# Optimization experiments

Measured on AMD Instinct MI355X. Metric: run time of the kernel, lower is better.

Reference implementation:

```python
import jax, jax.numpy as jnp
import numpy as np

B, T, C = 2, 2048, 2048
H, KV, D = 16, 4, 128   # n_head, n_kv_head, head_dim
EPS = 1.1920929e-07     # torch.finfo(float32).eps, F.rms_norm default


def setup_inputs() -> dict:
    key = jax.random.key(0)
    ks = jax.random.split(key, 7)
    x = jax.random.normal(ks[0], (B, T, C), dtype=jnp.float32)
    # rope angles: cos/sin of positions, broadcastable to [B,T,H,D//2]
    inv_freq = 1.0 / (10000.0 ** (jnp.arange(0, D // 2, dtype=jnp.float32) / (D // 2)))
    ang = jnp.arange(T, dtype=jnp.float32)[:, None] * inv_freq[None, :]
    cos = jnp.cos(ang)[None, :, None, :]  # [1,T,1,D/2]
    sin = jnp.sin(ang)[None, :, None, :]
    s = 0.02
    Wq = jax.random.normal(ks[1], (C, H * D), dtype=jnp.float32) * s
    Wk = jax.random.normal(ks[2], (C, KV * D), dtype=jnp.float32) * s
    Wv = jax.random.normal(ks[3], (C, KV * D), dtype=jnp.float32) * s
    Wo = jax.random.normal(ks[4], (C, C), dtype=jnp.float32) * s
    return {"x": x, "cos": cos, "sin": sin, "Wq": Wq, "Wk": Wk, "Wv": Wv, "Wo": Wo}


def _rope(t, cos, sin):
    d = t.shape[-1] // 2
    t1, t2 = t[..., :d], t[..., d:]
    return jnp.concatenate([t1 * cos + t2 * sin, -t1 * sin + t2 * cos], axis=-1)


def _rmsnorm(t):
    return t * jax.lax.rsqrt(jnp.mean(t * t, axis=-1, keepdims=True) + EPS)


def reference(x, cos, sin, Wq, Wk, Wv, Wo):
    q = (x @ Wq).reshape(B, T, H, D)
    k = (x @ Wk).reshape(B, T, KV, D)
    v = (x @ Wv).reshape(B, T, KV, D)
    q = _rmsnorm(_rope(q, cos, sin))
    k = _rmsnorm(_rope(k, cos, sin))
    # [B, KV, G, T, D] query grouped per kv head (GQA)
    G = H // KV
    qh = q.transpose(0, 2, 1, 3).reshape(B, KV, G, T, D)
    kh = k.transpose(0, 2, 1, 3)  # [B, KV, T, D]
    vh = v.transpose(0, 2, 1, 3)
    scale = 1.0 / np.sqrt(D).astype(np.float32)
    scores = jnp.einsum('bhgqd,bhkd->bhgqk', qh, kh) * scale
    causal = jnp.tril(jnp.ones((T, T), dtype=bool))
    scores = jnp.where(causal, scores, jnp.finfo(scores.dtype).min)
    attn = jax.nn.softmax(scores, axis=-1)
    y = jnp.einsum('bhgqk,bhkd->bhgqd', attn, vh)  # [B,KV,G,T,D]
    y = y.reshape(B, H, T, D).transpose(0, 2, 1, 3).reshape(B, T, C)
    return y @ Wo
```

## Files before the change

### kernel.cpp

```cpp
#include <hip/hip_runtime.h>

using bf16x8 = __attribute__((ext_vector_type(8))) short;
using f32x4  = __attribute__((ext_vector_type(4))) float;

#define B_  2
#define T_  2048
#define C_  2048
#define H_  16
#define KV_ 4
#define D_  128

__device__ __forceinline__ unsigned short f2b(float f) {
  union { float f; unsigned int u; } v; v.f = f;
  unsigned int r = v.u + 0x7fffu + ((v.u >> 16) & 1u);
  return (unsigned short)(r >> 16);
}
__device__ __forceinline__ float b2f(unsigned short u) {
  union { unsigned int u; float f; } v; v.u = ((unsigned int)u) << 16;
  return v.f;
}
__device__ __forceinline__ unsigned int cvt_pk_bf16(float lo, float hi) {
  unsigned int r;
  asm("v_cvt_pk_bf16_f32 %0, %1, %2" : "=v"(r) : "v"(lo), "v"(hi));
  return r;
}
__device__ __forceinline__ void gld_lds16(const void* g, void* l) {
  __builtin_amdgcn_global_load_lds(
      (__attribute__((address_space(1))) void*)g,
      (__attribute__((address_space(3))) void*)l, 16, 0, 0);
}

__global__ void prep(const float* __restrict__ x, unsigned short* __restrict__ xb,
                     const float* __restrict__ Wq, const float* __restrict__ Wk,
                     const float* __restrict__ Wv, const float* __restrict__ Wo,
                     unsigned short* __restrict__ Wqt, unsigned short* __restrict__ Wkt,
                     unsigned short* __restrict__ Wvt, unsigned short* __restrict__ Wot) {
  __shared__ float s[32][33];
  int bid = blockIdx.x, tid = threadIdx.x;
  if (bid < 8192) {
    int i = bid * 256 + tid;
    float4 f = ((const float4*)x)[i];
    ushort4 u; u.x = f2b(f.x); u.y = f2b(f.y); u.z = f2b(f.z); u.w = f2b(f.w);
    ((ushort4*)xb)[i] = u;
    return;
  }
  int id = bid - 8192;
  const float* W; unsigned short* Wt; int N;
  if (id < 4096)      { W = Wq; Wt = Wqt; N = 2048; }
  else if (id < 5120) { W = Wk; Wt = Wkt; N = 512;  id -= 4096; }
  else if (id < 6144) { W = Wv; Wt = Wvt; N = 512;  id -= 5120; }
  else                { W = Wo; Wt = Wot; N = 2048; id -= 6144; }
  int ntiles = N >> 5;
  int n0 = (id % ntiles) * 32, k0 = (id / ntiles) * 32;
  int tx = tid & 31, ty = tid >> 5;
  #pragma unroll
  for (int yy = 0; yy < 32; yy += 8)
    s[ty + yy][tx] = W[(size_t)(k0 + ty + yy) * N + n0 + tx];
  __syncthreads();
  #pragma unroll
  for (int yy = 0; yy < 32; yy += 8)
    Wt[(size_t)(n0 + ty + yy) * 2048 + k0 + tx] = f2b(s[tx][ty + yy]);
}

__global__ __launch_bounds__(512, 2) void qkv_gemm2p(
    const unsigned short* __restrict__ xb,
    const unsigned short* __restrict__ Wt,
    unsigned short* __restrict__ qkv) {
  __shared__ unsigned short lds[57344];

  const int id  = (int)blockIdx.x;
  const int xcd = id & 7, j = id >> 3;
  const int mt  = xcd * 2 + (j >> 4);
  const int nt  = j & 15;
  const int m0 = mt * 256, n0 = nt * 192;

  const int tid = (int)threadIdx.x;
  const int w = tid >> 6, lane = tid & 63;
  const int quad = lane >> 4, l16 = lane & 15;
  const int wr = w >> 1, wc = w & 1;
  const int swz = (l16 & 12) << 1;

  const unsigned short* Ab = xb + (size_t)m0 * 2048;
  const unsigned short* Bb = Wt + (size_t)n0 * 2048;

  int ar[4], axc[4];
  #pragma unroll
  for (int kq = 0; kq < 4; ++kq) {
    int ca = tid + kq * 512;
    ar[kq]  = (ca & 1023) >> 2;
    axc[kq] = ((ca & 3) * 8) ^ ((((ca & 1023) >> 4) & 3) << 3);
  }
  const int khb1 = (tid < 256) ? 0 : 1;
  int bidx[3] = { tid, tid + 512 - khb1 * 768, tid + 256 };
  int bkh[3]  = { 0, khb1, 1 };
  int br[3], bxc[3];
  #pragma unroll
  for (int kq = 0; kq < 3; ++kq) {
    br[kq]  = bidx[kq] >> 2;
    bxc[kq] = ((bidx[kq] & 3) * 8) ^ (((bidx[kq] >> 4) & 3) << 3);
  }

#define STAGE(buf, kb) do { \
    unsigned short* da_ = lds + (buf) * 16384; \
    _Pragma("unroll") \
    for (int kq = 0; kq < 4; ++kq) { \
      int ca_ = tid + kq * 512; \
      gld_lds16(Ab + (size_t)ar[kq] * 2048 + (kb) + (ca_ >> 10) * 32 + axc[kq], da_ + ca_ * 8); \
    } \
    unsigned short* db_ = lds + 32768 + (buf) * 12288; \
    _Pragma("unroll") \
    for (int kq = 0; kq < 3; ++kq) \
      gld_lds16(Bb + (size_t)br[kq] * 2048 + (kb) + bkh[kq] * 32 + bxc[kq], \
                db_ + bkh[kq] * 6144 + bidx[kq] * 8); \
  } while (0)

  f32x4 acc[4][6] = {};

  STAGE(0, 0);
  __syncthreads();

  const unsigned short* aB = lds + (wr * 64 + l16) * 32 + (quad * 8 ^ swz);
  const unsigned short* bB = lds + 32768 + (wc * 96 + l16) * 32 + (quad * 8 ^ swz);

  for (int t = 0; t < 32; ++t) {
    const int cur = t & 1;
    if (t < 31) STAGE(cur ^ 1, (t + 1) * 64);
    #pragma unroll
    for (int kh = 0; kh < 2; ++kh) {
      bf16x8 a[4], b[6];
      #pragma unroll
      for (int m = 0; m < 4; ++m)
        a[m] = *(const bf16x8*)(aB + cur * 16384 + kh * 8192 + m * 512);
      #pragma unroll
      for (int n = 0; n < 6; ++n)
        b[n] = *(const bf16x8*)(bB + cur * 12288 + kh * 6144 + n * 512);
      #pragma unroll
      for (int m = 0; m < 4; ++m)
        #pragma unroll
        for (int n = 0; n < 6; ++n)
          acc[m][n] = __builtin_amdgcn_mfma_f32_16x16x32_bf16(a[m], b[n], acc[m][n], 0, 0, 0);
    }
    __syncthreads();
  }
#undef STAGE

  #pragma unroll
  for (int m = 0; m < 4; ++m)
    #pragma unroll
    for (int r = 0; r < 4; ++r) {
      int row = m0 + wr * 64 + m * 16 + quad * 4 + r;
      #pragma unroll
      for (int n = 0; n < 6; ++n) {
        int col = n0 + wc * 96 + n * 16 + l16;
        qkv[(size_t)row * 3072 + col] = f2b(acc[m][n][r]);
      }
    }
}

__global__ __launch_bounds__(512, 2) void out_gemm2p(
    const unsigned short* __restrict__ yb,
    const unsigned short* __restrict__ Wot,
    float* __restrict__ out) {
  __shared__ unsigned short lds[49152];

  const int id  = (int)blockIdx.x;
  const int xcd = id & 7, j = id >> 3;
  const int mt  = xcd * 2 + (j >> 4);
  const int nt  = j & 15;
  const int m0 = mt * 256, n0 = nt * 128;

  const int tid = (int)threadIdx.x;
  const int w = tid >> 6, lane = tid & 63;
  const int quad = lane >> 4, l16 = lane & 15;
  const int wr = w >> 1, wc = w & 1;
  const int swz = (l16 & 12) << 1;

  const unsigned short* Ab = yb  + (size_t)m0 * 2048;
  const unsigned short* Bb = Wot + (size_t)n0 * 2048;

  int ar[4], axc[4];
  #pragma unroll
  for (int kq = 0; kq < 4; ++kq) {
    int ca = tid + kq * 512;
    ar[kq]  = (ca & 1023) >> 2;
    axc[kq] = ((ca & 3) * 8) ^ ((((ca & 1023) >> 4) & 3) << 3);
  }
  int brr[2], bxc[2];
  #pragma unroll
  for (int kq = 0; kq < 2; ++kq) {
    int cb = tid + kq * 512;
    brr[kq] = (cb & 511) >> 2;
    bxc[kq] = ((cb & 3) * 8) ^ ((((cb & 511) >> 4) & 3) << 3);
  }

#define STAGE(buf, kb) do { \
    unsigned short* da_ = lds + (buf) * 16384; \
    _Pragma("unroll") \
    for (int kq = 0; kq < 4; ++kq) { \
      int ca_ = tid + kq * 512; \
      gld_lds16(Ab + (size_t)ar[kq] * 2048 + (kb) + (ca_ >> 10) * 32 + axc[kq], da_ + ca_ * 8); \
    } \
    unsigned short* db_ = lds + 32768 + (buf) * 8192; \
    _Pragma("unroll") \
    for (int kq = 0; kq < 2; ++kq) { \
      int cb_ = tid + kq * 512; \
      gld_lds16(Bb + (size_t)brr[kq] * 2048 + (kb) + kq * 32 + bxc[kq], db_ + cb_ * 8); \
    } \
  } while (0)

  f32x4 acc[4][4] = {};

  STAGE(0, 0);
  __syncthreads();

  const unsigned short* aB = lds + (wr * 64 + l16) * 32 + (quad * 8 ^ swz);
  const unsigned short* bB = lds + 32768 + (wc * 64 + l16) * 32 + (quad * 8 ^ swz);

  for (int t = 0; t < 32; ++t) {
    const int cur = t & 1;
    if (t < 31) STAGE(cur ^ 1, (t + 1) * 64);
    #pragma unroll
    for (int kh = 0; kh < 2; ++kh) {
      bf16x8 a[4], b[4];
      #pragma unroll
      for (int m = 0; m < 4; ++m)
        a[m] = *(const bf16x8*)(aB + cur * 16384 + kh * 8192 + m * 512);
      #pragma unroll
      for (int n = 0; n < 4; ++n)
        b[n] = *(const bf16x8*)(bB + cur * 8192 + kh * 4096 + n * 512);
      #pragma unroll
      for (int m = 0; m < 4; ++m)
        #pragma unroll
        for (int n = 0; n < 4; ++n)
          acc[m][n] = __builtin_amdgcn_mfma_f32_16x16x32_bf16(a[m], b[n], acc[m][n], 0, 0, 0);
    }
    __syncthreads();
  }
#undef STAGE

  #pragma unroll
  for (int m = 0; m < 4; ++m)
    #pragma unroll
    for (int r = 0; r < 4; ++r) {
      int row = m0 + wr * 64 + m * 16 + quad * 4 + r;
      #pragma unroll
      for (int n = 0; n < 4; ++n) {
        int col = n0 + wc * 64 + n * 16 + l16;
        out[(size_t)row * 2048 + col] = acc[m][n][r];
      }
    }
}

template <int NH>
__device__ __forceinline__ void ropenorm_row(
    const unsigned short* __restrict__ in, const float* __restrict__ cs,
    const float* __restrict__ sn, unsigned short* __restrict__ out,
    float oscale, int off, int row, int lane) {
  int head = row % NH;
  int t = (row / NH) & (T_ - 1);
  int b = row / (NH * T_);
  const unsigned short* p = in + (size_t)(b * T_ + t) * 3072 + off + head * D_;
  unsigned int u  = *(const unsigned int*)(p + 2 * lane);
  unsigned int up = (unsigned int)__shfl_xor((int)u, 32, 64);
  int dh = (lane & 31) * 2;
  float2 c2 = ((const float2*)(cs + t * 64))[lane & 31];
  float2 s2 = ((const float2*)(sn + t * 64))[lane & 31];
  float a0 = b2f((unsigned short)(u & 0xffff)),  a1 = b2f((unsigned short)(u >> 16));
  float p0 = b2f((unsigned short)(up & 0xffff)), p1 = b2f((unsigned short)(up >> 16));
  float sgn = (lane < 32) ? 1.0f : -1.0f;
  float oa = a0 * c2.x + sgn * p0 * s2.x;
  float ob = a1 * c2.y + sgn * p1 * s2.y;
  float ss = oa * oa + ob * ob;
  #pragma unroll
  for (int off2 = 32; off2 > 0; off2 >>= 1) ss += __shfl_xor(ss, off2, 64);
  float r = rsqrtf(ss * (1.0f / 128.0f) + 1.1920929e-07f) * oscale;
  unsigned int outu = cvt_pk_bf16(oa * r, ob * r);
  size_t base = ((size_t)((b * NH + head) * 128 + (t >> 4))) * 2048 + (size_t)(t & 15) * 8;
  int f = ((lane < 32) ? 0 : 8) + (dh >> 3);
  *(unsigned int*)(out + base + (size_t)f * 128 + (dh & 7)) = outu;
}

__global__ void ropenorm_qk(const unsigned short* __restrict__ qkv,
                            const float* __restrict__ cs, const float* __restrict__ sn,
                            unsigned short* __restrict__ qfr,
                            unsigned short* __restrict__ kfr) {
  int bid = blockIdx.x;
  int lane = threadIdx.x & 63;
  int wv = threadIdx.x >> 6;
  if (bid < 16384) {
    ropenorm_row<16>(qkv, cs, sn, qfr, 0.08838834764831845f, 0, bid * 4 + wv, lane);
  } else {
    ropenorm_row<4>(qkv, cs, sn, kfr, 1.0f, 2048, (bid - 16384) * 4 + wv, lane);
  }
}

__global__ void vfrag_k(const unsigned short* __restrict__ qkv, unsigned short* __restrict__ vf) {
  int it = blockIdx.x;
  int b = blockIdx.y >> 2, kv = blockIdx.y & 3;
  int d = threadIdx.x, ty = threadIdx.y;
  int t0 = it * 64;
  size_t obase = ((size_t)((b * KV_ + kv) * 32 + it)) * 8192
               + (size_t)(d >> 4) * 1024 + (size_t)(d & 15) * 8;
  #pragma unroll
  for (int tcg = 0; tcg < 4; ++tcg) {
    int tc = ty * 4 + tcg;
    unsigned short val[8];
    #pragma unroll
    for (int e = 0; e < 8; ++e)
      val[e] = qkv[((size_t)(b * T_) + t0 + tc * 8 + e) * 3072 + 2560 + kv * D_ + d];
    ushort4 u0 = {val[0], val[1], val[2], val[3]};
    ushort4 u1 = {val[4], val[5], val[6], val[7]};
    *(ushort4*)(vf + obase + (size_t)tc * 128)     = u0;
    *(ushort4*)(vf + obase + (size_t)tc * 128 + 4) = u1;
  }
}

__global__ __launch_bounds__(512, 2) void attn_kernel(
    const unsigned short* __restrict__ qf, const unsigned short* __restrict__ kf,
    const unsigned short* __restrict__ vf, unsigned short* __restrict__ yb) {
  __shared__ __align__(16) char smem[135168];
  unsigned short* kls = (unsigned short*)smem;
  unsigned short* vls = (unsigned short*)(smem + 65536);
  unsigned short* Pls = (unsigned short*)(smem + 98304);

  const int xp = (int)blockIdx.x, b = xp >> 2, kv = xp & 3;
  const int jy = (int)blockIdx.y;
  const int tid = (int)threadIdx.x;
  const int w = tid >> 6, lane = tid & 63;
  const int quad = lane >> 4, l16 = lane & 15;
  const int hh = w & 3, half = w >> 2;
  const int h = kv * 4 + hh;
  unsigned short* myP = Pls + w * (32 * 72);

  const unsigned short* Kf = kf + (size_t)(b * KV_ + kv) * 128 * 2048;
  const unsigned short* Vf = vf + (size_t)(b * KV_ + kv) * 32 * 8192;

  const int swl = quad << 4;
  const int cs0 = (tid * 8) ^ swl;
  const int cs1 = ((tid + 512) * 8) ^ swl;
  const int cd0 = tid * 8, cd1 = tid * 8 + 4096;

#define STAGE_K(buf, it0) do { \
    const unsigned short* s_ = Kf + (size_t)(it0) * 8192; \
    unsigned short* d_ = kls + (buf) * 16384; \
    gld_lds16(s_ + cs0, d_ + cd0);               gld_lds16(s_ + cs1, d_ + cd1); \
    gld_lds16(s_ + 8192 + cs0, d_ + 8192 + cd0); gld_lds16(s_ + 8192 + cs1, d_ + 8192 + cd1); \
  } while (0)
#define STAGE_V(it0) do { \
    const unsigned short* s_ = Vf + (size_t)(it0) * 8192; \
    gld_lds16(s_ + cs0, vls + cd0);               gld_lds16(s_ + cs1, vls + cd1); \
    gld_lds16(s_ + 8192 + cs0, vls + 8192 + cd0); gld_lds16(s_ + 8192 + cs1, vls + 8192 + cd1); \
  } while (0)

  for (int ph = 0; ph < 2; ++ph) {
    const int qt = ph ? (63 - jy) : jy;
    const int q0 = qt * 32;
    const int ntile = (qt >> 1) + 1;
    const int R = (ntile + 1) >> 1;

    const unsigned short* Qf = qf + ((size_t)(b * H_ + h) * 128 + qt * 2) * 2048;
    bf16x8 bq[2][4];
    #pragma unroll
    for (int i = 0; i < 2; ++i)
      #pragma unroll
      for (int kk = 0; kk < 4; ++kk)
        bq[i][kk] = *(const bf16x8*)(Qf + (size_t)i * 2048 + (kk * 4 + quad) * 128 + l16 * 8);

    float l_i[2] = {0.f, 0.f};
    f32x4 o[2][8] = {};

    STAGE_K(0, 0);

    for (int r = 0; r < R; ++r) {
      const int cur = r & 1;
      const bool more = (r + 1 < R);
      STAGE_V(2 * r);
      if (more) STAGE_K(cur ^ 1, 2 * r + 2);
      if (more) asm volatile("s_waitcnt vmcnt(8)" ::: "memory");
      else      asm volatile("s_waitcnt vmcnt(4)" ::: "memory");
      __builtin_amdgcn_s_barrier();

      const int it = 2 * r + half;
      const bool active = it < ntile;
      f32x4 sc[4][2] = {};
      if (active) {
        const unsigned short* kb = kls + cur * 16384 + half * 8192;
        #pragma unroll
        for (int kk = 0; kk < 4; ++kk) {
          bf16x8 ak[4];
          #pragma unroll
          for (int jt = 0; jt < 4; ++jt)
            ak[jt] = *(const bf16x8*)(kb + ((jt * 2048 + (kk * 4 + quad) * 128 + l16 * 8) ^ swl));
          #pragma unroll
          for (int jt = 0; jt < 4; ++jt)
            #pragma unroll
            for (int i = 0; i < 2; ++i)
              sc[jt][i] = __builtin_amdgcn_mfma_f32_16x16x32_bf16(ak[jt], bq[i][kk], sc[jt][i], 0, 0, 0);
        }
        if (it == ntile - 1) {
          #pragma unroll
          for (int jt = 0; jt < 4; ++jt) {
            int kg = it * 64 + jt * 16 + quad * 4;
            #pragma unroll
            for (int i = 0; i < 2; ++i) {
              int qg = q0 + i * 16 + l16;
              #pragma unroll
              for (int rr = 0; rr < 4; ++rr)
                if (kg + rr > qg) sc[jt][i][rr] = -3.0e38f;
            }
          }
        }
        #pragma unroll
        for (int i = 0; i < 2; ++i) {
          float part = 0.f;
          #pragma unroll
          for (int jt = 0; jt < 4; ++jt)
            #pragma unroll
            for (int rr = 0; rr < 4; ++rr) {
              float p = __expf(sc[jt][i][rr] - 12.0f);
              sc[jt][i][rr] = p; part += p;
            }
          l_i[i] += part;
        }
        #pragma unroll
        for (int i = 0; i < 2; ++i)
          #pragma unroll
          for (int jt = 0; jt < 4; ++jt) {
            uint2 uu;
            uu.x = cvt_pk_bf16(sc[jt][i][0], sc[jt][i][1]);
            uu.y = cvt_pk_bf16(sc[jt][i][2], sc[jt][i][3]);
            *(uint2*)(myP + (i * 16 + l16) * 72 + jt * 16 + quad * 4) = uu;
          }
      }

      if (more) asm volatile("s_waitcnt vmcnt(4)" ::: "memory");
      else      asm volatile("s_waitcnt vmcnt(0)" ::: "memory");
      __builtin_amdgcn_s_barrier();

      if (active) {
        const unsigned short* vb = vls + half * 8192;
        #pragma unroll
        for (int kk2 = 0; kk2 < 2; ++kk2) {
          bf16x8 ap[2], bv2[8];
          #pragma unroll
          for (int i = 0; i < 2; ++i)
            ap[i] = *(const bf16x8*)(myP + (i * 16 + l16) * 72 + kk2 * 32 + quad * 8);
          #pragma unroll
          for (int jj = 0; jj < 8; ++jj)
            bv2[jj] = *(const bf16x8*)(vb + ((jj * 1024 + (kk2 * 4 + quad) * 128 + l16 * 8) ^ swl));
          #pragma unroll
          for (int i = 0; i < 2; ++i)
            #pragma unroll
            for (int jj = 0; jj < 8; ++jj)
              o[i][jj] = __builtin_amdgcn_mfma_f32_16x16x32_bf16(ap[i], bv2[jj], o[i][jj], 0, 0, 0);
        }
      }
      __builtin_amdgcn_s_barrier();
    }

    float lsum[2];
    #pragma unroll
    for (int i = 0; i < 2; ++i) {
      float l = l_i[i];
      l += __shfl_xor(l, 16, 64);
      l += __shfl_xor(l, 32, 64);
      lsum[i] = l;
    }

    __syncthreads();
    float* oc = (float*)smem + hh * 4256;
    float* lc = oc + 32 * 132;
    if (half == 1) {
      #pragma unroll
      for (int i = 0; i < 2; ++i) {
        if (quad == 0) lc[i * 16 + l16] = lsum[i];
        #pragma unroll
        for (int jj = 0; jj < 8; ++jj)
          #pragma unroll
          for (int rr = 0; rr < 4; ++rr)
            oc[(i * 16 + quad * 4 + rr) * 132 + jj * 16 + l16] = o[i][jj][rr];
      }
    }
    __syncthreads();
    if (half == 0) {
      #pragma unroll
      for (int i = 0; i < 2; ++i) {
        float l = lsum[i] + lc[i * 16 + l16];
        float linv = 1.0f / l;
        float lr[4];
        #pragma unroll
        for (int rr = 0; rr < 4; ++rr) lr[rr] = __shfl(linv, quad * 4 + rr, 64);
        #pragma unroll
        for (int rr = 0; rr < 4; ++rr) {
          int tg = q0 + i * 16 + quad * 4 + rr;
          unsigned short* yr = yb + (((size_t)(b * T_ + tg)) * H_ + h) * D_;
          #pragma unroll
          for (int jj = 0; jj < 8; ++jj) {
            float vsum = o[i][jj][rr] + oc[(i * 16 + quad * 4 + rr) * 132 + jj * 16 + l16];
            yr[jj * 16 + l16] = f2b(vsum * lr[rr]);
          }
        }
      }
    }
    __syncthreads();
  }
#undef STAGE_K
#undef STAGE_V
}

extern "C" void kernel_launch(void* const* d_in, const int* in_sizes, int n_in,
                              void* d_out, int out_size, void* d_ws, size_t ws_size,
                              hipStream_t stream) {
  (void)in_sizes; (void)n_in; (void)out_size; (void)ws_size;
  const float* x  = (const float*)d_in[0];
  const float* cs = (const float*)d_in[1];
  const float* sn = (const float*)d_in[2];
  const float* Wq = (const float*)d_in[3];
  const float* Wk = (const float*)d_in[4];
  const float* Wv = (const float*)d_in[5];
  const float* Wo = (const float*)d_in[6];
  float* out = (float*)d_out;
  char* ws = (char*)d_ws;

  unsigned short* xb     = (unsigned short*)(ws + 0);
  unsigned short* Wqkvt  = (unsigned short*)(ws + 16777216);
  unsigned short* Wot    = (unsigned short*)(ws + 29360128);
  unsigned short* qkvcat = (unsigned short*)(ws + 37748736);
  unsigned short* qfr    = (unsigned short*)(ws + 62914560);
  unsigned short* kfr    = (unsigned short*)(ws + 79691776);
  unsigned short* vfr    = (unsigned short*)(ws + 83886080);
  unsigned short* yb     = xb;

  prep<<<dim3(18432), dim3(256), 0, stream>>>(
      x, xb, Wq, Wk, Wv, Wo,
      Wqkvt, Wqkvt + (size_t)2048 * 2048, Wqkvt + (size_t)2560 * 2048, Wot);
  qkv_gemm2p<<<dim3(256), dim3(512), 0, stream>>>(xb, Wqkvt, qkvcat);
  ropenorm_qk<<<dim3(20480), dim3(256), 0, stream>>>(qkvcat, cs, sn, qfr, kfr);
  vfrag_k<<<dim3(32, 8), dim3(128, 2), 0, stream>>>(qkvcat, vfr);
  attn_kernel<<<dim3(8, 32), dim3(512), 0, stream>>>(qfr, kfr, vfr, yb);
  out_gemm2p<<<dim3(256), dim3(512), 0, stream>>>(yb, Wot, out);
}
```

Measured before the change: 282.1 us.

## Use fragment-ordered LDS layout in GEMMs and fuse V fragment kernel into rope

Both GEMM kernels now stage tiles into LDS in MFMA fragment order: each 16-row group stores its k-chunks contiguously, so a wave's fragment read is a contiguous 1 KiB block. This replaces the XOR swizzle and is meant to cut LDS bank conflicts and address arithmetic. The global load pattern changes as a result, and coalescing may suffer. Separately, the V fragment repacking kernel is merged into the rope/norm kernel as extra blocks, which removes one kernel launch.

```diff
diff --git a/kernel.cpp b/kernel.cpp
--- a/kernel.cpp
+++ b/kernel.cpp
@@ -78,40 +78,34 @@
   const int w = tid >> 6, lane = tid & 63;
   const int quad = lane >> 4, l16 = lane & 15;
   const int wr = w >> 1, wc = w & 1;
-  const int swz = (l16 & 12) << 1;
 
   const unsigned short* Ab = xb + (size_t)m0 * 2048;
   const unsigned short* Bb = Wt + (size_t)n0 * 2048;
 
-  int ar[4], axc[4];
+  int arow[4], aoff[4];
   #pragma unroll
   for (int kq = 0; kq < 4; ++kq) {
-    int ca = tid + kq * 512;
-    ar[kq]  = (ca & 1023) >> 2;
-    axc[kq] = ((ca & 3) * 8) ^ ((((ca & 1023) >> 4) & 3) << 3);
-  }
-  const int khb1 = (tid < 256) ? 0 : 1;
-  int bidx[3] = { tid, tid + 512 - khb1 * 768, tid + 256 };
-  int bkh[3]  = { 0, khb1, 1 };
-  int br[3], bxc[3];
+    int c = tid + kq * 512;
+    arow[kq] = (c >> 7) * 16 + (c & 15);
+    aoff[kq] = ((c >> 6) & 1) * 32 + ((c >> 4) & 3) * 8;
+  }
+  int brow[3], boff[3];
   #pragma unroll
   for (int kq = 0; kq < 3; ++kq) {
-    br[kq]  = bidx[kq] >> 2;
-    bxc[kq] = ((bidx[kq] & 3) * 8) ^ (((bidx[kq] >> 4) & 3) << 3);
+    int c = tid + kq * 512;
+    brow[kq] = (c >> 7) * 16 + (c & 15);
+    boff[kq] = ((c >> 6) & 1) * 32 + ((c >> 4) & 3) * 8;
   }
 
 #define STAGE(buf, kb) do { \
     unsigned short* da_ = lds + (buf) * 16384; \
     _Pragma("unroll") \
-    for (int kq = 0; kq < 4; ++kq) { \
-      int ca_ = tid + kq * 512; \
-      gld_lds16(Ab + (size_t)ar[kq] * 2048 + (kb) + (ca_ >> 10) * 32 + axc[kq], da_ + ca_ * 8); \
-    } \
+    for (int kq = 0; kq < 4; ++kq) \
+      gld_lds16(Ab + (size_t)arow[kq] * 2048 + (kb) + aoff[kq], da_ + (tid + kq * 512) * 8); \
     unsigned short* db_ = lds + 32768 + (buf) * 12288; \
     _Pragma("unroll") \
     for (int kq = 0; kq < 3; ++kq) \
-      gld_lds16(Bb + (size_t)br[kq] * 2048 + (kb) + bkh[kq] * 32 + bxc[kq], \
-                db_ + bkh[kq] * 6144 + bidx[kq] * 8); \
+      gld_lds16(Bb + (size_t)brow[kq] * 2048 + (kb) + boff[kq], db_ + (tid + kq * 512) * 8); \
   } while (0)
 
   f32x4 acc[4][6] = {};
@@ -119,8 +113,8 @@
   STAGE(0, 0);
   __syncthreads();
 
-  const unsigned short* aB = lds + (wr * 64 + l16) * 32 + (quad * 8 ^ swz);
-  const unsigned short* bB = lds + 32768 + (wc * 96 + l16) * 32 + (quad * 8 ^ swz);
+  const unsigned short* aB = lds + (wr * 4) * 1024 + quad * 128 + l16 * 8;
+  const unsigned short* bB = lds + 32768 + (wc * 6) * 1024 + quad * 128 + l16 * 8;
 
   for (int t = 0; t < 32; ++t) {
     const int cur = t & 1;
@@ -130,10 +124,10 @@
       bf16x8 a[4], b[6];
       #pragma unroll
       for (int m = 0; m < 4; ++m)
-        a[m] = *(const bf16x8*)(aB + cur * 16384 + kh * 8192 + m * 512);
+        a[m] = *(const bf16x8*)(aB + cur * 16384 + m * 1024 + kh * 512);
       #pragma unroll
       for (int n = 0; n < 6; ++n)
-        b[n] = *(const bf16x8*)(bB + cur * 12288 + kh * 6144 + n * 512);
+        b[n] = *(const bf16x8*)(bB + cur * 12288 + n * 1024 + kh * 512);
       #pragma unroll
       for (int m = 0; m < 4; ++m)
         #pragma unroll
@@ -173,39 +167,34 @@
   const int w = tid >> 6, lane = tid & 63;
   const int quad = lane >> 4, l16 = lane & 15;
   const int wr = w >> 1, wc = w & 1;
-  const int swz = (l16 & 12) << 1;
 
   const unsigned short* Ab = yb  + (size_t)m0 * 2048;
   const unsigned short* Bb = Wot + (size_t)n0 * 2048;
 
-  int ar[4], axc[4];
+  int arow[4], aoff[4];
   #pragma unroll
   for (int kq = 0; kq < 4; ++kq) {
-    int ca = tid + kq * 512;
-    ar[kq]  = (ca & 1023) >> 2;
-    axc[kq] = ((ca & 3) * 8) ^ ((((ca & 1023) >> 4) & 3) << 3);
-  }
-  int brr[2], bxc[2];
+    int c = tid + kq * 512;
+    arow[kq] = (c >> 7) * 16 + (c & 15);
+    aoff[kq] = ((c >> 6) & 1) * 32 + ((c >> 4) & 3) * 8;
+  }
+  int brow[2], boff[2];
   #pragma unroll
   for (int kq = 0; kq < 2; ++kq) {
-    int cb = tid + kq * 512;
-    brr[kq] = (cb & 511) >> 2;
-    bxc[kq] = ((cb & 3) * 8) ^ ((((cb & 511) >> 4) & 3) << 3);
+    int c = tid + kq * 512;
+    brow[kq] = (c >> 7) * 16 + (c & 15);
+    boff[kq] = ((c >> 6) & 1) * 32 + ((c >> 4) & 3) * 8;
   }
 
 #define STAGE(buf, kb) do { \
     unsigned short* da_ = lds + (buf) * 16384; \
     _Pragma("unroll") \
-    for (int kq = 0; kq < 4; ++kq) { \
-      int ca_ = tid + kq * 512; \
-      gld_lds16(Ab + (size_t)ar[kq] * 2048 + (kb) + (ca_ >> 10) * 32 + axc[kq], da_ + ca_ * 8); \
-    } \
+    for (int kq = 0; kq < 4; ++kq) \
+      gld_lds16(Ab + (size_t)arow[kq] * 2048 + (kb) + aoff[kq], da_ + (tid + kq * 512) * 8); \
     unsigned short* db_ = lds + 32768 + (buf) * 8192; \
     _Pragma("unroll") \
-    for (int kq = 0; kq < 2; ++kq) { \
-      int cb_ = tid + kq * 512; \
-      gld_lds16(Bb + (size_t)brr[kq] * 2048 + (kb) + kq * 32 + bxc[kq], db_ + cb_ * 8); \
-    } \
+    for (int kq = 0; kq < 2; ++kq) \
+      gld_lds16(Bb + (size_t)brow[kq] * 2048 + (kb) + boff[kq], db_ + (tid + kq * 512) * 8); \
   } while (0)
 
   f32x4 acc[4][4] = {};
@@ -213,8 +202,8 @@
   STAGE(0, 0);
   __syncthreads();
 
-  const unsigned short* aB = lds + (wr * 64 + l16) * 32 + (quad * 8 ^ swz);
-  const unsigned short* bB = lds + 32768 + (wc * 64 + l16) * 32 + (quad * 8 ^ swz);
+  const unsigned short* aB = lds + (wr * 4) * 1024 + quad * 128 + l16 * 8;
+  const unsigned short* bB = lds + 32768 + (wc * 4) * 1024 + quad * 128 + l16 * 8;
 
   for (int t = 0; t < 32; ++t) {
     const int cur = t & 1;
@@ -224,10 +213,10 @@
       bf16x8 a[4], b[4];
       #pragma unroll
       for (int m = 0; m < 4; ++m)
-        a[m] = *(const bf16x8*)(aB + cur * 16384 + kh * 8192 + m * 512);
+        a[m] = *(const bf16x8*)(aB + cur * 16384 + m * 1024 + kh * 512);
       #pragma unroll
       for (int n = 0; n < 4; ++n)
-        b[n] = *(const bf16x8*)(bB + cur * 8192 + kh * 4096 + n * 512);
+        b[n] = *(const bf16x8*)(bB + cur * 8192 + n * 1024 + kh * 512);
       #pragma unroll
       for (int m = 0; m < 4; ++m)
         #pragma unroll
@@ -280,24 +269,24 @@
   *(unsigned int*)(out + base + (size_t)f * 128 + (dh & 7)) = outu;
 }
 
-__global__ void ropenorm_qk(const unsigned short* __restrict__ qkv,
-                            const float* __restrict__ cs, const float* __restrict__ sn,
-                            unsigned short* __restrict__ qfr,
-                            unsigned short* __restrict__ kfr) {
-  int bid = blockIdx.x;
-  int lane = threadIdx.x & 63;
-  int wv = threadIdx.x >> 6;
+__global__ void post_k(const unsigned short* __restrict__ qkv,
+                       const float* __restrict__ cs, const float* __restrict__ sn,
+                       unsigned short* __restrict__ qfr, unsigned short* __restrict__ kfr,
+                       unsigned short* __restrict__ vf) {
+  int bid = blockIdx.x, tid = threadIdx.x;
+  int lane = tid & 63, wv = tid >> 6;
   if (bid < 16384) {
     ropenorm_row<16>(qkv, cs, sn, qfr, 0.08838834764831845f, 0, bid * 4 + wv, lane);
-  } else {
+    return;
+  }
+  if (bid < 20480) {
     ropenorm_row<4>(qkv, cs, sn, kfr, 1.0f, 2048, (bid - 16384) * 4 + wv, lane);
-  }
-}
-
-__global__ void vfrag_k(const unsigned short* __restrict__ qkv, unsigned short* __restrict__ vf) {
-  int it = blockIdx.x;
-  int b = blockIdx.y >> 2, kv = blockIdx.y & 3;
-  int d = threadIdx.x, ty = threadIdx.y;
+    return;
+  }
+  int id = bid - 20480;
+  int it = id & 31, y = id >> 5;
+  int b = y >> 2, kv = y & 3;
+  int d = tid & 127, ty = tid >> 7;
   int t0 = it * 64;
   size_t obase = ((size_t)((b * KV_ + kv) * 32 + it)) * 8192
                + (size_t)(d >> 4) * 1024 + (size_t)(d & 15) * 8;
@@ -535,8 +524,7 @@
       x, xb, Wq, Wk, Wv, Wo,
       Wqkvt, Wqkvt + (size_t)2048 * 2048, Wqkvt + (size_t)2560 * 2048, Wot);
   qkv_gemm2p<<<dim3(256), dim3(512), 0, stream>>>(xb, Wqkvt, qkvcat);
-  ropenorm_qk<<<dim3(20480), dim3(256), 0, stream>>>(qkvcat, cs, sn, qfr, kfr);
-  vfrag_k<<<dim3(32, 8), dim3(128, 2), 0, stream>>>(qkvcat, vfr);
+  post_k<<<dim3(20736), dim3(256), 0, stream>>>(qkvcat, cs, sn, qfr, kfr, vfr);
   attn_kernel<<<dim3(8, 32), dim3(512), 0, stream>>>(qfr, kfr, vfr, yb);
   out_gemm2p<<<dim3(256), dim3(512), 0, stream>>>(yb, Wot, out);
 }
```

After: 326.3 us. 1.16x slower.
